# Optimization experiments

Hardware: AMD Instinct MI355X
Metric: run time of the kernel (lower is better)

The kernel has to match this reference:

```python
import jax, jax.numpy as jnp
import numpy as np
from jax import lax

DIM = 64
K = 3
GROUPS = 1
NUM_KERNELS = 4
B, H, W = 32, 128, 128


def setup_inputs() -> dict:
    key = jax.random.key(0)
    k1, k2, k3, k4 = jax.random.split(key, 4)
    x = jax.random.normal(k1, (B, DIM, H, W), dtype=jnp.float32)
    attention = jax.random.uniform(k2, (B, NUM_KERNELS), dtype=jnp.float32)
    # kaiming-uniform-like init per kernel: bound = sqrt(6 / fan_in)
    fan_in = (DIM // GROUPS) * K * K
    bound = float(np.sqrt(6.0 / fan_in))
    weight = jax.random.uniform(k3, (NUM_KERNELS, DIM, DIM // GROUPS, K, K),
                                dtype=jnp.float32, minval=-bound, maxval=bound)
    bias_p = jax.random.normal(k4, (NUM_KERNELS, DIM), dtype=jnp.float32) * 0.1
    return {"x": x, "attention": attention, "weight": weight, "bias_p": bias_p}


def reference(x, attention, weight, bias_p):
    # Mix kernel bank per sample: [B, nk] @ [nk, dim*dim//g*k*k]
    w_flat = weight.reshape(NUM_KERNELS, -1)
    w_mix = (attention @ w_flat).reshape(B, DIM, DIM // GROUPS, K, K)
    b_mix = attention @ bias_p  # [B, dim]

    def conv_one(xb, wb, bb):
        # xb: [C,H,W], wb: [C_out, C_in//g, k, k]
        out = lax.conv_general_dilated(
            xb[None], wb, window_strides=(1, 1), padding="SAME",
            dimension_numbers=("NCHW", "OIHW", "NCHW"),
            feature_group_count=GROUPS)
        return out[0] + bb[:, None, None]

    return jax.vmap(conv_one)(x, w_mix, b_mix)  # [B, dim, H, W]
```

## Files before the change

### kernel.cpp

```cpp
#include <hip/hip_runtime.h>


#define DIM 64
#define BATCH 32
#define HH 128
#define WW 128
#define NK 4

typedef __attribute__((ext_vector_type(4))) float f32x4;
typedef __attribute__((ext_vector_type(8))) short bf16x8;
typedef __attribute__((ext_vector_type(8))) unsigned short ushort8;
typedef __attribute__((ext_vector_type(2))) unsigned int u32x2;

static __device__ __forceinline__ unsigned short f2bf(float f) {
    union { float f; unsigned u; } v; v.f = f;
    unsigned r = v.u + 0x7fffu + ((v.u >> 16) & 1u);
    return (unsigned short)(r >> 16);
}
static __device__ __forceinline__ unsigned pack2(float a, float b) {
    return (unsigned)f2bf(a) | ((unsigned)f2bf(b) << 16);
}

__global__ __launch_bounds__(256) void mix_weights(
    const float* __restrict__ w, const float* __restrict__ att,
    unsigned short* __restrict__ wmix) {
    __shared__ float tr[4][576];
    int wave = threadIdx.x >> 6, lane = threadIdx.x & 63;
    int idx = blockIdx.x * 4 + wave;
    int b = idx >> 6, co = idx & 63;
    float a[NK];
    #pragma unroll
    for (int k = 0; k < NK; ++k) a[k] = att[b * NK + k];
    float s[9];
    #pragma unroll
    for (int t = 0; t < 9; ++t) s[t] = 0.f;
    #pragma unroll
    for (int k = 0; k < NK; ++k) {
        const float* wp = w + (size_t)(k * DIM + co) * 576;
        #pragma unroll
        for (int t = 0; t < 9; ++t)
            s[t] += a[k] * wp[t * 64 + lane];
    }
    #pragma unroll
    for (int t = 0; t < 9; ++t) tr[wave][t * 64 + lane] = s[t];
    __syncthreads();
    int mt = co >> 4;
    int lo = ((lane >> 3) & 3) * 16 + (co & 15);
    int ss = lane >> 5;
    int jj = lane & 7;
    #pragma unroll
    for (int t = 0; t < 9; ++t) {
        float v = tr[wave][lane * 9 + t];
        wmix[(size_t)((((b * 9 + t) * 2 + ss) * 4 + mt) * 64 + lo) * 8 + jj] = f2bf(v);
    }
}

__global__ __launch_bounds__(256) void mix_bias(
    const float* __restrict__ bias, const float* __restrict__ att,
    float* __restrict__ bmix) {
    int idx = blockIdx.x * 256 + threadIdx.x;
    if (idx >= BATCH * DIM) return;
    int b = idx >> 6, co = idx & 63;
    float s = 0.f;
    for (int k = 0; k < NK; ++k) s += att[b * NK + k] * bias[k * DIM + co];
    bmix[idx] = s;
}

__global__ __launch_bounds__(256, 3) void conv_mfma(
    const float* __restrict__ x, const unsigned short* __restrict__ wmix,
    const float* __restrict__ bmix, float* __restrict__ out) {

    __shared__ unsigned short Xs[6 * 66 * 64];

    int bid = blockIdx.x;
    bid = (bid & 7) * 256 + (bid >> 3);
    int b   = bid >> 6;
    int r6  = bid & 63;
    int h0  = (r6 >> 1) * 4;
    int w0  = (r6 & 1) * 64;

    int tid  = threadIdx.x;
    int wave = tid >> 6, lane = tid & 63;
    int l15  = lane & 15, q = lane >> 4;

    const unsigned short* wa = wmix + (size_t)b * 9 * 4096;
    bf16x8 afp[3][4];
    #pragma unroll
    for (int u0 = 0; u0 < 3; ++u0)
        #pragma unroll
        for (int mt = 0; mt < 4; ++mt)
            afp[u0][mt] = *(const bf16x8*)&wa[(size_t)((u0 * 4 + mt) * 64 + lane) * 8];

    int cq = tid >> 4, c4 = tid & 15;
    #pragma unroll
    for (int half = 0; half < 2; ++half) {
        f32x4 xv[3][4];
        #pragma unroll
        for (int rr = 0; rr < 3; ++rr) {
            int r = half * 3 + rr;
            int hin = h0 - 1 + r;
            bool ok = (hin >= 0) && (hin < HH);
            #pragma unroll
            for (int i = 0; i < 4; ++i) {
                f32x4 z = {0.f, 0.f, 0.f, 0.f};
                xv[rr][i] = ok ? *(const f32x4*)&x[(((size_t)b * DIM + 4 * cq + i) * HH + hin) * WW + w0 + 4 * c4] : z;
            }
        }
        #pragma unroll
        for (int rr = 0; rr < 3; ++rr) {
            int r = half * 3 + rr;
            #pragma unroll
            for (int j = 0; j < 4; ++j) {
                int c = 4 * c4 + 1 + j;
                u32x2 pk;
                pk.x = pack2(xv[rr][0][j], xv[rr][1][j]);
                pk.y = pack2(xv[rr][2][j], xv[rr][3][j]);
                int xi = (r * 66 + c) * 64 + (((cq >> 1) ^ ((c >> 1) & 7)) << 3) + 4 * (cq & 1);
                *(u32x2*)&Xs[xi] = pk;
            }
        }
    }
    #pragma unroll
    for (int e = 0; e < 3; ++e) {
        int item = e * 256 + tid;
        int edge = item >= 384;
        int jj = item - edge * 384;
        int ci = jj & 63, r = jj >> 6;
        int hin = h0 - 1 + r;
        int win = edge ? (w0 + 64) : (w0 - 1);
        float v = 0.f;
        if (hin >= 0 && hin < HH && win >= 0 && win < WW)
            v = x[(((size_t)b * DIM + ci) * HH + hin) * WW + win];
        int c = edge ? 65 : 0;
        Xs[(r * 66 + c) * 64 + (((ci >> 3) ^ ((c >> 1) & 7)) << 3) + (ci & 7)] = f2bf(v);
    }

    f32x4 acc[4][4];
    f32x4 zero = {0.f, 0.f, 0.f, 0.f};
    #pragma unroll
    for (int mt = 0; mt < 4; ++mt)
        #pragma unroll
        for (int nt = 0; nt < 4; ++nt) acc[mt][nt] = zero;

    __syncthreads();

    #pragma unroll
    for (int u = 0; u < 18; ++u) {
        int tap = u >> 1, s = u & 1;
        int kh = tap / 3, kw = tap - kh * 3;
        int r = wave + kh;
        int g = s * 4 + q;
        bf16x8 bfr[4];
        #pragma unroll
        for (int nt = 0; nt < 4; ++nt) {
            int c = nt * 16 + l15 + kw;
            bfr[nt] = *(const bf16x8*)&Xs[(r * 66 + c) * 64 + ((g ^ ((c >> 1) & 7)) << 3)];
        }
        #pragma unroll
        for (int mt = 0; mt < 4; ++mt)
            #pragma unroll
            for (int nt = 0; nt < 4; ++nt)
                acc[mt][nt] = __builtin_amdgcn_mfma_f32_16x16x32_bf16(
                    afp[u % 3][mt], bfr[nt], acc[mt][nt], 0, 0, 0);
        if (u + 3 < 18) {
            #pragma unroll
            for (int mt = 0; mt < 4; ++mt)
                afp[u % 3][mt] = *(const bf16x8*)&wa[(size_t)(((u + 3) * 4 + mt) * 64 + lane) * 8];
        }
    }

    float biasr[4][4];
    #pragma unroll
    for (int mt = 0; mt < 4; ++mt)
        #pragma unroll
        for (int rg = 0; rg < 4; ++rg)
            biasr[mt][rg] = bmix[b * DIM + mt * 16 + q * 4 + rg];
    int h = h0 + wave;
    #pragma unroll
    for (int mt = 0; mt < 4; ++mt) {
        #pragma unroll
        for (int nt = 0; nt < 4; ++nt) {
            int wcol = w0 + nt * 16 + l15;
            #pragma unroll
            for (int rg = 0; rg < 4; ++rg) {
                int co = mt * 16 + q * 4 + rg;
                out[(((size_t)b * DIM + co) * HH + h) * WW + wcol] = acc[mt][nt][rg] + biasr[mt][rg];
            }
        }
    }
}

extern "C" void kernel_launch(void* const* d_in, const int* in_sizes, int n_in,
                              void* d_out, int out_size, void* d_ws, size_t ws_size,
                              hipStream_t stream) {
    const float* x   = (const float*)d_in[0];
    const float* att = (const float*)d_in[1];
    const float* wgt = (const float*)d_in[2];
    const float* bia = (const float*)d_in[3];
    float* out = (float*)d_out;

    unsigned short* wmix = (unsigned short*)d_ws;
    float* bmix = (float*)((char*)d_ws + 2359296);

    mix_weights<<<512, 256, 0, stream>>>(wgt, att, wmix);
    mix_bias<<<8, 256, 0, stream>>>(bia, att, bmix);
    conv_mfma<<<2048, 256, 0, stream>>>(x, wmix, bmix, out);
}
```

Measured before the change: 271.8 us.

## Stream 16 output rows per block through a rolling 8-row LDS ring buffer

Each block now computes 16 output rows instead of 4, cutting the grid from 2048 to 512 blocks. Input rows are held in a circular 8-row shared buffer, so the halo rows are loaded once and not re-read by neighbouring blocks. The next four rows are prefetched from global memory into registers during the MFMA loop and written into the ring buffer partway through and after it. This aims to cut redundant halo loads and per-block setup, and to overlap global loads with compute. In exchange it uses more LDS and registers, lowers occupancy to 2 blocks per CU, and leaves fewer blocks to spread across the CUs.

```diff
diff --git a/kernel.cpp b/kernel.cpp
--- a/kernel.cpp
+++ b/kernel.cpp
@@ -9,7 +9,6 @@
 
 typedef __attribute__((ext_vector_type(4))) float f32x4;
 typedef __attribute__((ext_vector_type(8))) short bf16x8;
-typedef __attribute__((ext_vector_type(8))) unsigned short ushort8;
 typedef __attribute__((ext_vector_type(2))) unsigned int u32x2;
 
 static __device__ __forceinline__ unsigned short f2bf(float f) {
@@ -18,7 +17,10 @@
     return (unsigned short)(r >> 16);
 }
 static __device__ __forceinline__ unsigned pack2(float a, float b) {
-    return (unsigned)f2bf(a) | ((unsigned)f2bf(b) << 16);
+    union { float f; unsigned u; } va, vb; va.f = a; vb.f = b;
+    unsigned ra = (va.u + 0x7fffu + ((va.u >> 16) & 1u)) >> 16;
+    unsigned rb = (vb.u + 0x7fffu + ((vb.u >> 16) & 1u)) >> 16;
+    return ra | (rb << 16);
 }
 
 __global__ __launch_bounds__(256) void mix_weights(
@@ -66,24 +68,26 @@
     bmix[idx] = s;
 }
 
-__global__ __launch_bounds__(256, 3) void conv_mfma(
+__global__ __launch_bounds__(256, 2) void conv_mfma(
     const float* __restrict__ x, const unsigned short* __restrict__ wmix,
     const float* __restrict__ bmix, float* __restrict__ out) {
 
-    __shared__ unsigned short Xs[6 * 66 * 64];
+    __shared__ unsigned short Xs[8 * 66 * 64];
 
     int bid = blockIdx.x;
-    bid = (bid & 7) * 256 + (bid >> 3);
-    int b   = bid >> 6;
-    int r6  = bid & 63;
-    int h0  = (r6 >> 1) * 4;
-    int w0  = (r6 & 1) * 64;
+    bid = (bid & 7) * 64 + (bid >> 3);
+    int b  = bid >> 4;
+    int wh = (bid >> 3) & 1;
+    int ch = bid & 7;
+    int h0 = ch * 16, w0 = wh * 64;
 
     int tid  = threadIdx.x;
     int wave = tid >> 6, lane = tid & 63;
     int l15  = lane & 15, q = lane >> 4;
+    int cq   = tid >> 4, c4 = tid & 15;
 
     const unsigned short* wa = wmix + (size_t)b * 9 * 4096;
+
     bf16x8 afp[3][4];
     #pragma unroll
     for (int u0 = 0; u0 < 3; ++u0)
@@ -91,14 +95,18 @@
         for (int mt = 0; mt < 4; ++mt)
             afp[u0][mt] = *(const bf16x8*)&wa[(size_t)((u0 * 4 + mt) * 64 + lane) * 8];
 
-    int cq = tid >> 4, c4 = tid & 15;
-    #pragma unroll
-    for (int half = 0; half < 2; ++half) {
-        f32x4 xv[3][4];
-        #pragma unroll
-        for (int rr = 0; rr < 3; ++rr) {
-            int r = half * 3 + rr;
-            int hin = h0 - 1 + r;
+    float biasr[4][4];
+    #pragma unroll
+    for (int mt = 0; mt < 4; ++mt)
+        #pragma unroll
+        for (int rg = 0; rg < 4; ++rg)
+            biasr[mt][rg] = bmix[b * DIM + mt * 16 + q * 4 + rg];
+
+    {
+        f32x4 xv[6][4];
+        #pragma unroll
+        for (int rr = 0; rr < 6; ++rr) {
+            int hin = h0 - 1 + rr;
             bool ok = (hin >= 0) && (hin < HH);
             #pragma unroll
             for (int i = 0; i < 4; ++i) {
@@ -106,33 +114,42 @@
                 xv[rr][i] = ok ? *(const f32x4*)&x[(((size_t)b * DIM + 4 * cq + i) * HH + hin) * WW + w0 + 4 * c4] : z;
             }
         }
-        #pragma unroll
-        for (int rr = 0; rr < 3; ++rr) {
-            int r = half * 3 + rr;
+        float ev[3];
+        #pragma unroll
+        for (int e = 0; e < 3; ++e) {
+            int item = e * 256 + tid;
+            int edge = item >= 384;
+            int jj = item - edge * 384;
+            int ci = jj & 63, rr = jj >> 6;
+            int hin = h0 - 1 + rr;
+            int win = edge ? (w0 + 64) : (w0 - 1);
+            float v = 0.f;
+            if (hin >= 0 && hin < HH && win >= 0 && win < WW)
+                v = x[(((size_t)b * DIM + ci) * HH + hin) * WW + win];
+            ev[e] = v;
+        }
+        #pragma unroll
+        for (int rr = 0; rr < 6; ++rr) {
+            int s = (rr + 7) & 7;
             #pragma unroll
             for (int j = 0; j < 4; ++j) {
                 int c = 4 * c4 + 1 + j;
                 u32x2 pk;
                 pk.x = pack2(xv[rr][0][j], xv[rr][1][j]);
                 pk.y = pack2(xv[rr][2][j], xv[rr][3][j]);
-                int xi = (r * 66 + c) * 64 + (((cq >> 1) ^ ((c >> 1) & 7)) << 3) + 4 * (cq & 1);
-                *(u32x2*)&Xs[xi] = pk;
-            }
-        }
-    }
-    #pragma unroll
-    for (int e = 0; e < 3; ++e) {
-        int item = e * 256 + tid;
-        int edge = item >= 384;
-        int jj = item - edge * 384;
-        int ci = jj & 63, r = jj >> 6;
-        int hin = h0 - 1 + r;
-        int win = edge ? (w0 + 64) : (w0 - 1);
-        float v = 0.f;
-        if (hin >= 0 && hin < HH && win >= 0 && win < WW)
-            v = x[(((size_t)b * DIM + ci) * HH + hin) * WW + win];
-        int c = edge ? 65 : 0;
-        Xs[(r * 66 + c) * 64 + (((ci >> 3) ^ ((c >> 1) & 7)) << 3) + (ci & 7)] = f2bf(v);
+                *(u32x2*)&Xs[(s * 66 + c) * 64 + (((cq >> 1) ^ ((c >> 1) & 7)) << 3) + 4 * (cq & 1)] = pk;
+            }
+        }
+        #pragma unroll
+        for (int e = 0; e < 3; ++e) {
+            int item = e * 256 + tid;
+            int edge = item >= 384;
+            int jj = item - edge * 384;
+            int ci = jj & 63, rr = jj >> 6;
+            int s = (rr + 7) & 7;
+            int c = edge ? 65 : 0;
+            Xs[(s * 66 + c) * 64 + (((ci >> 3) ^ ((c >> 1) & 7)) << 3) + (ci & 7)] = f2bf(ev[e]);
+        }
     }
 
     f32x4 acc[4][4];
@@ -145,46 +162,115 @@
     __syncthreads();
 
     #pragma unroll
-    for (int u = 0; u < 18; ++u) {
-        int tap = u >> 1, s = u & 1;
-        int kh = tap / 3, kw = tap - kh * 3;
-        int r = wave + kh;
-        int g = s * 4 + q;
-        bf16x8 bfr[4];
-        #pragma unroll
-        for (int nt = 0; nt < 4; ++nt) {
-            int c = nt * 16 + l15 + kw;
-            bfr[nt] = *(const bf16x8*)&Xs[(r * 66 + c) * 64 + ((g ^ ((c >> 1) & 7)) << 3)];
-        }
-        #pragma unroll
-        for (int mt = 0; mt < 4; ++mt)
-            #pragma unroll
-            for (int nt = 0; nt < 4; ++nt)
-                acc[mt][nt] = __builtin_amdgcn_mfma_f32_16x16x32_bf16(
-                    afp[u % 3][mt], bfr[nt], acc[mt][nt], 0, 0, 0);
-        if (u + 3 < 18) {
+    for (int t = 0; t < 4; ++t) {
+        f32x4 nx[4][4];
+        float ne[2];
+        if (t < 3) {
+            #pragma unroll
+            for (int rr = 0; rr < 4; ++rr) {
+                int hin = h0 + 4 * t + 5 + rr;
+                bool ok = (hin < HH);
+                #pragma unroll
+                for (int i = 0; i < 4; ++i) {
+                    f32x4 z = {0.f, 0.f, 0.f, 0.f};
+                    nx[rr][i] = ok ? *(const f32x4*)&x[(((size_t)b * DIM + 4 * cq + i) * HH + hin) * WW + w0 + 4 * c4] : z;
+                }
+            }
+            #pragma unroll
+            for (int e = 0; e < 2; ++e) {
+                int item = e * 256 + tid;
+                int rr = item >> 7, side = (item >> 6) & 1, ci = item & 63;
+                int hin = h0 + 4 * t + 5 + rr;
+                int win = side ? (w0 + 64) : (w0 - 1);
+                float v = 0.f;
+                if (hin < HH && win >= 0 && win < WW)
+                    v = x[(((size_t)b * DIM + ci) * HH + hin) * WW + win];
+                ne[e] = v;
+            }
+        }
+
+        #pragma unroll
+        for (int st = 0; st < 18; ++st) {
+            int tap = st >> 1, sgrp = st & 1;
+            int kh = tap / 3, kw = tap - kh * 3;
+            int r = (4 * t + 7 + wave + kh) & 7;
+            int g = sgrp * 4 + q;
+            bf16x8 bfr[4];
+            #pragma unroll
+            for (int nt = 0; nt < 4; ++nt) {
+                int c = nt * 16 + l15 + kw;
+                bfr[nt] = *(const bf16x8*)&Xs[(r * 66 + c) * 64 + ((g ^ ((c >> 1) & 7)) << 3)];
+            }
             #pragma unroll
             for (int mt = 0; mt < 4; ++mt)
-                afp[u % 3][mt] = *(const bf16x8*)&wa[(size_t)(((u + 3) * 4 + mt) * 64 + lane) * 8];
-        }
-    }
-
-    float biasr[4][4];
-    #pragma unroll
-    for (int mt = 0; mt < 4; ++mt)
-        #pragma unroll
-        for (int rg = 0; rg < 4; ++rg)
-            biasr[mt][rg] = bmix[b * DIM + mt * 16 + q * 4 + rg];
-    int h = h0 + wave;
-    #pragma unroll
-    for (int mt = 0; mt < 4; ++mt) {
-        #pragma unroll
-        for (int nt = 0; nt < 4; ++nt) {
-            int wcol = w0 + nt * 16 + l15;
-            #pragma unroll
-            for (int rg = 0; rg < 4; ++rg) {
-                int co = mt * 16 + q * 4 + rg;
-                out[(((size_t)b * DIM + co) * HH + h) * WW + wcol] = acc[mt][nt][rg] + biasr[mt][rg];
+                #pragma unroll
+                for (int nt = 0; nt < 4; ++nt)
+                    acc[mt][nt] = __builtin_amdgcn_mfma_f32_16x16x32_bf16(
+                        afp[st % 3][mt], bfr[nt], acc[mt][nt], 0, 0, 0);
+            #pragma unroll
+            for (int mt = 0; mt < 4; ++mt)
+                afp[st % 3][mt] = *(const bf16x8*)&wa[(size_t)((((st + 3) % 18) * 4 + mt) * 64 + lane) * 8];
+
+            if (st == 8 && t < 3) {
+                #pragma unroll
+                for (int rr = 0; rr < 2; ++rr) {
+                    int s = (4 * t + 5 + rr) & 7;
+                    #pragma unroll
+                    for (int j = 0; j < 4; ++j) {
+                        int c = 4 * c4 + 1 + j;
+                        u32x2 pk;
+                        pk.x = pack2(nx[rr][0][j], nx[rr][1][j]);
+                        pk.y = pack2(nx[rr][2][j], nx[rr][3][j]);
+                        *(u32x2*)&Xs[(s * 66 + c) * 64 + (((cq >> 1) ^ ((c >> 1) & 7)) << 3) + 4 * (cq & 1)] = pk;
+                    }
+                }
+                {
+                    int item = tid;
+                    int rr = item >> 7, side = (item >> 6) & 1, ci = item & 63;
+                    int s = (4 * t + 5 + rr) & 7;
+                    int c = side ? 65 : 0;
+                    Xs[(s * 66 + c) * 64 + (((ci >> 3) ^ ((c >> 1) & 7)) << 3) + (ci & 7)] = f2bf(ne[0]);
+                }
+            }
+        }
+
+        __syncthreads();
+
+        if (t < 3) {
+            #pragma unroll
+            for (int rr = 2; rr < 4; ++rr) {
+                int s = (4 * t + 5 + rr) & 7;
+                #pragma unroll
+                for (int j = 0; j < 4; ++j) {
+                    int c = 4 * c4 + 1 + j;
+                    u32x2 pk;
+                    pk.x = pack2(nx[rr][0][j], nx[rr][1][j]);
+                    pk.y = pack2(nx[rr][2][j], nx[rr][3][j]);
+                    *(u32x2*)&Xs[(s * 66 + c) * 64 + (((cq >> 1) ^ ((c >> 1) & 7)) << 3) + 4 * (cq & 1)] = pk;
+                }
+            }
+            {
+                int item = 256 + tid;
+                int rr = item >> 7, side = (item >> 6) & 1, ci = item & 63;
+                int s = (4 * t + 5 + rr) & 7;
+                int c = side ? 65 : 0;
+                Xs[(s * 66 + c) * 64 + (((ci >> 3) ^ ((c >> 1) & 7)) << 3) + (ci & 7)] = f2bf(ne[1]);
+            }
+            __syncthreads();
+        }
+
+        int h = h0 + 4 * t + wave;
+        #pragma unroll
+        for (int mt = 0; mt < 4; ++mt) {
+            #pragma unroll
+            for (int nt = 0; nt < 4; ++nt) {
+                int wcol = w0 + nt * 16 + l15;
+                #pragma unroll
+                for (int rg = 0; rg < 4; ++rg) {
+                    int co = mt * 16 + q * 4 + rg;
+                    out[(((size_t)b * DIM + co) * HH + h) * WW + wcol] = acc[mt][nt][rg] + biasr[mt][rg];
+                }
+                acc[mt][nt] = zero;
             }
         }
     }
@@ -204,5 +290,5 @@
 
     mix_weights<<<512, 256, 0, stream>>>(wgt, att, wmix);
     mix_bias<<<8, 256, 0, stream>>>(bia, att, bmix);
-    conv_mfma<<<2048, 256, 0, stream>>>(x, wmix, bmix, out);
-}
+    conv_mfma<<<512, 256, 0, stream>>>(x, wmix, bmix, out);
+}
```

After: 384.8 us. 41.6% more time.
